# Kernel optimization log

Measured on AMD Instinct MI355X. Metric: run time of the kernel, lower is better.

The kernel has to match this reference:

```python
import math
import jax, jax.numpy as jnp
import numpy as np

NUM_HEADS = 12
EPS = 1e-4


def softmax_kernel_features(data, proj, is_query):
    # data: [B,H,N,d], proj: [m,d] -> features [B,H,N,m]
    d = data.shape[-1]
    data_normalizer = 1.0 / math.sqrt(math.sqrt(d))
    ratio = 1.0 / math.sqrt(proj.shape[0])
    data_dash = jnp.einsum('bhnd,md->bhnm', data_normalizer * data, proj)
    diag_data = (jnp.sum(jnp.square(data), axis=-1, keepdims=True)
                 * 0.5 * data_normalizer * data_normalizer)  # [B,H,N,1]
    if is_query:
        stab = jnp.max(data_dash, axis=-1, keepdims=True)
    else:
        stab = jnp.max(data_dash)
    return ratio * (jnp.exp(data_dash - diag_data - stab) + EPS)


def setup_inputs() -> dict:
    key = jax.random.key(0)
    k0, k1, k2, k3, k4 = jax.random.split(key, 5)
    B, N, C, H = 8, 4096, 768, NUM_HEADS
    hd = C // H
    m = int(hd * math.log(hd))  # 266
    x = jax.random.normal(k0, (B, N, C), dtype=jnp.float32)
    W_qkv = jax.random.normal(k1, (C, 3 * C), dtype=jnp.float32) / math.sqrt(C)
    W_proj = jax.random.normal(k2, (C, C), dtype=jnp.float32) / math.sqrt(C)
    b_proj = jnp.zeros((C,), dtype=jnp.float32)
    proj_mat = jax.random.normal(k3, (m, hd), dtype=jnp.float32)
    return {'x': x, 'W_qkv': W_qkv, 'W_proj': W_proj, 'b_proj': b_proj,
            'proj_mat': proj_mat}


def reference(x, W_qkv, W_proj, b_proj, proj_mat):
    B, N, C = x.shape
    H = NUM_HEADS
    hd = C // H
    qkv = (x @ W_qkv).reshape(B, N, 3, H, hd)
    qkv = jnp.transpose(qkv, (2, 0, 3, 1, 4))  # [3,B,H,N,hd]
    q, k, v = qkv[0], qkv[1], qkv[2]
    q1 = softmax_kernel_features(q, proj_mat, is_query=True)   # [B,H,N,m]
    k1 = softmax_kernel_features(k, proj_mat, is_query=False)  # [B,H,N,m]
    # FAVOR+ non-causal linear attention
    kv = jnp.einsum('bhnm,bhnd->bhmd', k1, v)        # [B,H,m,hd]
    ksum = jnp.sum(k1, axis=2)                        # [B,H,m]
    z = 1.0 / jnp.einsum('bhnm,bhm->bhn', q1, ksum)  # [B,H,N]
    out = jnp.einsum('bhnm,bhmd->bhnd', q1, kv) * z[..., None]
    out = jnp.transpose(out, (0, 2, 1, 3)).reshape(B, N, C)
    return out @ W_proj + b_proj
```

## Files before the change

### kernel.cpp

```cpp
#include <hip/hip_runtime.h>
#include <hip/hip_bf16.h>
#include <math.h>

#define B_ 8
#define N_TOK 4096
#define C_ 768
#define H_ 12
#define HD_ 64
#define M_ 266
#define TC_ 2304
#define BH_ 96
#define ROWS_ 32768

#define M2 288
#define MP 296
#define KVS 72

#define DN 0.35355339059327373f
#define RATIO 0.06131393394849658f
#define FEPS 1e-4f
#define NEG_INF -3.0e38f

typedef __attribute__((ext_vector_type(4))) float f32x4;
typedef __attribute__((ext_vector_type(8))) short bf16x8;

__device__ __forceinline__ float bf2f(unsigned short u) {
  return __uint_as_float(((unsigned int)u) << 16);
}
__device__ __forceinline__ unsigned short f2bf(float f) {
  unsigned int x = __float_as_uint(f);
  unsigned int r = (x + 0x7fffu + ((x >> 16) & 1u)) >> 16;
  return (unsigned short)r;
}

#define GLOAD_LDS16(g, l) \
  __builtin_amdgcn_global_load_lds( \
      (const __attribute__((address_space(1))) void*)(g), \
      (__attribute__((address_space(3))) void*)(l), 16, 0, 0)

__global__ __launch_bounds__(256) void cast_bf16(
    const float* __restrict__ src, unsigned short* __restrict__ dst, int n)
{
  int i = (blockIdx.x * 256 + threadIdx.x) * 4;
  if (i < n) {
    float4 v = *(const float4*)&src[i];
    ushort4 u;
    u.x = f2bf(v.x); u.y = f2bf(v.y); u.z = f2bf(v.z); u.w = f2bf(v.w);
    *(ushort4*)&dst[i] = u;
  }
}

__global__ __launch_bounds__(256) void cast_pbf(
    const float* __restrict__ P, unsigned short* __restrict__ Pbf)
{
  int idx = blockIdx.x * 256 + threadIdx.x;
  if (idx < M2 * 64) {
    int m = idx >> 6;
    Pbf[idx] = (m < M_) ? f2bf(P[idx]) : (unsigned short)0;
  }
}

__global__ __launch_bounds__(256) void transpose_cast(
    const float* __restrict__ src, unsigned short* __restrict__ dst,
    int R, int Ccols)
{
  __shared__ float t[32][33];
  const int c0 = blockIdx.x * 32, r0 = blockIdx.y * 32;
  const int tx = threadIdx.x & 31, ty = threadIdx.x >> 5;
#pragma unroll
  for (int i = 0; i < 32; i += 8)
    t[ty + i][tx] = src[(size_t)(r0 + ty + i) * Ccols + c0 + tx];
  __syncthreads();
#pragma unroll
  for (int i = 0; i < 32; i += 8)
    dst[(size_t)(c0 + ty + i) * R + r0 + tx] = f2bf(t[tx][ty + i]);
}

template <int NT, int C_BF16, int HAS_BIAS>
__global__ __launch_bounds__(512) void gemm_pipe(
    const unsigned short* __restrict__ A, const unsigned short* __restrict__ Bt,
    const float* __restrict__ bias, void* __restrict__ Cptr)
{
  __shared__ unsigned short lds_[73728];
  const int Kdim = 768, Ndim = NT * 128;
  const int tid = threadIdx.x;
  const int lane = tid & 63, w = tid >> 6;

  const int id = blockIdx.x;
  const int sid = (id & 7) * (16 * NT) + (id >> 3);
  const int row0 = (sid / NT) * 256;
  const int col0 = (sid % NT) * 128;

  const int srow = w * 8 + (lane >> 3);
  const int skb = (((lane & 7) ^ ((lane >> 3) & 7)) << 4);
  const size_t agb0 = (size_t)(row0 + srow) * Kdim + (skb >> 1);
  const size_t agb1 = (size_t)(row0 + 64 + srow) * Kdim + (skb >> 1);
  const size_t agb2 = (size_t)(row0 + 128 + srow) * Kdim + (skb >> 1);
  const size_t agb3 = (size_t)(row0 + 192 + srow) * Kdim + (skb >> 1);
  const size_t bgb0 = (size_t)(col0 + srow) * Kdim + (skb >> 1);
  const size_t bgb1 = (size_t)(col0 + 64 + srow) * Kdim + (skb >> 1);
  const int al0 = 0 * 4096 + w * 512 + lane * 8;
  const int al1 = 1 * 4096 + w * 512 + lane * 8;
  const int al2 = 2 * 4096 + w * 512 + lane * 8;
  const int al3 = 3 * 4096 + w * 512 + lane * 8;
  const int bl0 = 16384 + 0 * 4096 + w * 512 + lane * 8;
  const int bl1 = 16384 + 1 * 4096 + w * 512 + lane * 8;

#define STAGE_Q(tt) do { \
    unsigned short* Lq_ = lds_ + ((tt) % 3) * 24576; \
    const int kq_ = (tt) * 64; \
    GLOAD_LDS16(A + agb0 + kq_, Lq_ + al0); \
    GLOAD_LDS16(A + agb1 + kq_, Lq_ + al1); \
    GLOAD_LDS16(A + agb2 + kq_, Lq_ + al2); \
    GLOAD_LDS16(A + agb3 + kq_, Lq_ + al3); \
    GLOAD_LDS16(Bt + bgb0 + kq_, Lq_ + bl0); \
    GLOAD_LDS16(Bt + bgb1 + kq_, Lq_ + bl1); \
  } while (0)

  const int fr = lane & 15, q = lane >> 4;
  const int wm = w >> 2, wn = w & 3;
  const int f7 = fr & 7;
  const int sl0 = ((q + 0) ^ f7) << 3;
  const int sl1 = ((q + 4) ^ f7) << 3;
  const int abase = (wm * 128 + fr) * 64;
  const int bbase0 = 16384 + (wn * 32 + fr) * 64;
  const int bbase1 = 16384 + (wn * 32 + 16 + fr) * 64;

  f32x4 acc[8][2];
  const f32x4 fz = {0.f, 0.f, 0.f, 0.f};
#pragma unroll
  for (int m = 0; m < 8; ++m) { acc[m][0] = fz; acc[m][1] = fz; }

  STAGE_Q(0);
  STAGE_Q(1);

#pragma unroll 1
  for (int t = 0; t < 12; ++t) {
    if (t < 10) STAGE_Q(t + 2);
    if (t < 10)       asm volatile("s_waitcnt vmcnt(12)" ::: "memory");
    else if (t == 10) asm volatile("s_waitcnt vmcnt(6)" ::: "memory");
    else              asm volatile("s_waitcnt vmcnt(0)" ::: "memory");
    __builtin_amdgcn_sched_barrier(0);
    __builtin_amdgcn_s_barrier();
    __builtin_amdgcn_sched_barrier(0);

    const unsigned short* Lb = lds_ + (t % 3) * 24576;
#pragma unroll
    for (int ks = 0; ks < 2; ++ks) {
      const int sl = ks ? sl1 : sl0;
      bf16x8 bv0 = *(const bf16x8*)&Lb[bbase0 + sl];
      bf16x8 bv1 = *(const bf16x8*)&Lb[bbase1 + sl];
      bf16x8 av[8];
#pragma unroll
      for (int m = 0; m < 8; ++m)
        av[m] = *(const bf16x8*)&Lb[abase + m * 1024 + sl];
      __builtin_amdgcn_s_setprio(1);
#pragma unroll
      for (int m = 0; m < 8; ++m) {
        acc[m][0] = __builtin_amdgcn_mfma_f32_16x16x32_bf16(av[m], bv0, acc[m][0], 0, 0, 0);
        acc[m][1] = __builtin_amdgcn_mfma_f32_16x16x32_bf16(av[m], bv1, acc[m][1], 0, 0, 0);
      }
      __builtin_amdgcn_s_setprio(0);
    }
    __builtin_amdgcn_sched_barrier(0);
    __builtin_amdgcn_s_barrier();
    __builtin_amdgcn_sched_barrier(0);
  }
#undef STAGE_Q

  const int orow = q * 4;
#pragma unroll
  for (int m = 0; m < 8; ++m) {
#pragma unroll
    for (int n = 0; n < 2; ++n) {
      const int c = col0 + wn * 32 + n * 16 + fr;
      float badd = 0.f;
      if constexpr (HAS_BIAS) badd = bias[c];
#pragma unroll
      for (int j = 0; j < 4; ++j) {
        const int r = row0 + wm * 128 + m * 16 + orow + j;
        float v = acc[m][n][j] + badd;
        if constexpr (C_BF16)
          ((unsigned short*)Cptr)[(size_t)r * Ndim + c] = f2bf(v);
        else
          ((float*)Cptr)[(size_t)r * Ndim + c] = v;
      }
    }
  }
}

__global__ __launch_bounds__(256) void kmax_mfma(
    const unsigned short* __restrict__ qkv, const unsigned short* __restrict__ Pbf,
    float* __restrict__ bmax)
{
  __shared__ unsigned short K_lds[2][64 * KVS];
  __shared__ float red[4];
  const int tid = threadIdx.x;
  const int w = tid >> 6, lane = tid & 63;
  const int lr = lane & 15, q = lane >> 4;
  const int bh = blockIdx.x, chunk = blockIdx.y;
  const int b = bh / H_, h = bh % H_;
  const int ms = w * 4;
  const int mc = (w == 3) ? 5 : 4;
  const int sn = 16 * w + (lane >> 2);
  const int sd0 = (lane & 3) * 16;
  const f32x4 fz = {0.f, 0.f, 0.f, 0.f};
  float mx = NEG_INF;

  bf16x8 pf0[5], pf1[5];
#pragma unroll
  for (int i = 0; i < 5; ++i) {
    const unsigned short* prow = Pbf + (size_t)((ms + i) * 16 + lr) * 64 + q * 8;
    pf0[i] = *(const bf16x8*)prow;
    pf1[i] = *(const bf16x8*)(prow + 32);
  }

  const unsigned short* kbase = qkv + (size_t)(b * N_TOK + chunk * 512 + sn) * TC_ + C_ + h * HD_ + sd0;
  const size_t gstep = (size_t)64 * TC_;

  int4 ka = *(const int4*)kbase;
  int4 kb = *(const int4*)(kbase + 8);
  *(int4*)&K_lds[0][sn * KVS + sd0] = ka;
  *(int4*)&K_lds[0][sn * KVS + sd0 + 8] = kb;
  asm volatile("s_waitcnt lgkmcnt(0)" ::: "memory");
  __builtin_amdgcn_s_barrier();

#pragma unroll 1
  for (int g = 0; g < 8; ++g) {
    const unsigned short* Kc = K_lds[g & 1];
    if (g < 7) {
      const unsigned short* kr = kbase + (size_t)(g + 1) * gstep;
      ka = *(const int4*)kr;
      kb = *(const int4*)(kr + 8);
    }
    __builtin_amdgcn_sched_barrier(0);
    bf16x8 bk[4][2];
#pragma unroll
    for (int nt = 0; nt < 4; ++nt) {
      bk[nt][0] = *(const bf16x8*)&Kc[(nt * 16 + lr) * KVS + q * 8];
      bk[nt][1] = *(const bf16x8*)&Kc[(nt * 16 + lr) * KVS + 32 + q * 8];
    }
#pragma unroll
    for (int i = 0; i < 5; ++i) {
      if (i >= mc) continue;
      const int m = (ms + i) * 16 + lr;
#pragma unroll
      for (int nt = 0; nt < 4; ++nt) {
        f32x4 s = fz;
        s = __builtin_amdgcn_mfma_f32_16x16x32_bf16(bk[nt][0], pf0[i], s, 0, 0, 0);
        s = __builtin_amdgcn_mfma_f32_16x16x32_bf16(bk[nt][1], pf1[i], s, 0, 0, 0);
        if (m < M_)
          mx = fmaxf(mx, fmaxf(fmaxf(s[0], s[1]), fmaxf(s[2], s[3])));
      }
    }
    if (g < 7) {
      __builtin_amdgcn_sched_barrier(0);
      unsigned short* Kn = (unsigned short*)K_lds[(g & 1) ^ 1];
      *(int4*)&Kn[sn * KVS + sd0] = ka;
      *(int4*)&Kn[sn * KVS + sd0 + 8] = kb;
      asm volatile("s_waitcnt lgkmcnt(0)" ::: "memory");
      __builtin_amdgcn_sched_barrier(0);
      __builtin_amdgcn_s_barrier();
      __builtin_amdgcn_sched_barrier(0);
    }
  }
#pragma unroll
  for (int off = 32; off >= 1; off >>= 1) mx = fmaxf(mx, __shfl_xor(mx, off));
  if (lane == 0) red[w] = mx;
  __syncthreads();
  if (tid == 0)
    bmax[chunk * BH_ + bh] = fmaxf(fmaxf(red[0], red[1]), fmaxf(red[2], red[3]));
}

__global__ __launch_bounds__(256) void kmax_reduce(
    const float* __restrict__ bmax, float* __restrict__ kmaxp, int n)
{
  __shared__ float red[4];
  float v = NEG_INF;
  for (int i = threadIdx.x; i < n; i += 256) v = fmaxf(v, bmax[i]);
#pragma unroll
  for (int off = 32; off >= 1; off >>= 1) v = fmaxf(v, __shfl_xor(v, off));
  if ((threadIdx.x & 63) == 0) red[threadIdx.x >> 6] = v;
  __syncthreads();
  if (threadIdx.x == 0)
    kmaxp[0] = DN * fmaxf(fmaxf(red[0], red[1]), fmaxf(red[2], red[3]));
}

__global__ __launch_bounds__(256) void kv_partial_mfma(
    const unsigned short* __restrict__ qkv, const unsigned short* __restrict__ Pbf,
    const float* __restrict__ kmaxp,
    float* __restrict__ kvpart, float* __restrict__ ksumpart)
{
  __shared__ unsigned short K_lds[2][64 * KVS];
  __shared__ unsigned short Vt_lds[2][64 * KVS];
  __shared__ unsigned short k1_lds[272 * KVS];
  __shared__ float diag_lds[2][64];
  const int tid = threadIdx.x;
  const int w = tid >> 6, lane = tid & 63;
  const int lr = lane & 15, q = lane >> 4;
  const int bh = blockIdx.x, chunk = blockIdx.y;
  const int b = bh / H_, h = bh % H_;
  const float stab = kmaxp[0];
  const int ms = w * 4;
  const int mc = (w == 3) ? 5 : 4;
  const int sn = 16 * w + (lane >> 2);
  const int sd0 = (lane & 3) * 16;
  const f32x4 fz = {0.f, 0.f, 0.f, 0.f};

  f32x4 kvacc[5][4];
  float ksacc[5];
#pragma unroll
  for (int i = 0; i < 5; ++i) {
    ksacc[i] = 0.f;
#pragma unroll
    for (int dt = 0; dt < 4; ++dt) kvacc[i][dt] = fz;
  }

  bf16x8 pf0[5], pf1[5];
#pragma unroll
  for (int i = 0; i < 5; ++i) {
    const unsigned short* prow = Pbf + (size_t)((ms + i) * 16 + lr) * 64 + q * 8;
    pf0[i] = *(const bf16x8*)prow;
    pf1[i] = *(const bf16x8*)(prow + 32);
  }

  const unsigned short* kbase = qkv + (size_t)(b * N_TOK + chunk * 512 + sn) * TC_ + C_ + h * HD_ + sd0;
  const size_t gstep = (size_t)64 * TC_;

  auto write_buf = [&](int bsel, int4 wka, int4 wkb, int4 wva, int4 wvb) {
    *(int4*)&K_lds[bsel][sn * KVS + sd0] = wka;
    *(int4*)&K_lds[bsel][sn * KVS + sd0 + 8] = wkb;
    float sq = 0.f;
    const unsigned short* pk0 = (const unsigned short*)&wka;
#pragma unroll
    for (int j = 0; j < 8; ++j) { float f = bf2f(pk0[j]); sq = fmaf(f, f, sq); }
    const unsigned short* pk1 = (const unsigned short*)&wkb;
#pragma unroll
    for (int j = 0; j < 8; ++j) { float f = bf2f(pk1[j]); sq = fmaf(f, f, sq); }
    sq += __shfl_xor(sq, 1);
    sq += __shfl_xor(sq, 2);
    if ((lane & 3) == 0) diag_lds[bsel][sn] = 0.0625f * sq;
    const unsigned short* pv0 = (const unsigned short*)&wva;
    const unsigned short* pv1 = (const unsigned short*)&wvb;
#pragma unroll
    for (int j = 0; j < 8; ++j) Vt_lds[bsel][(sd0 + j) * KVS + sn] = pv0[j];
#pragma unroll
    for (int j = 0; j < 8; ++j) Vt_lds[bsel][(sd0 + 8 + j) * KVS + sn] = pv1[j];
  };

  int4 ka = *(const int4*)kbase;
  int4 kb = *(const int4*)(kbase + 8);
  int4 va = *(const int4*)(kbase + C_);
  int4 vb = *(const int4*)(kbase + C_ + 8);
  write_buf(0, ka, kb, va, vb);
  asm volatile("s_waitcnt lgkmcnt(0)" ::: "memory");
  __builtin_amdgcn_s_barrier();

#pragma unroll 1
  for (int g = 0; g < 8; ++g) {
    const int cur = g & 1;
    const unsigned short* Kc = K_lds[cur];
    const unsigned short* Vc = Vt_lds[cur];
    const float* Dc = diag_lds[cur];
    if (g < 7) {
      const unsigned short* kr = kbase + (size_t)(g + 1) * gstep;
      ka = *(const int4*)kr;
      kb = *(const int4*)(kr + 8);
      va = *(const int4*)(kr + C_);
      vb = *(const int4*)(kr + C_ + 8);
    }
    __builtin_amdgcn_sched_barrier(0);

    bf16x8 bk[4][2];
#pragma unroll
    for (int nt = 0; nt < 4; ++nt) {
      bk[nt][0] = *(const bf16x8*)&Kc[(nt * 16 + lr) * KVS + q * 8];
      bk[nt][1] = *(const bf16x8*)&Kc[(nt * 16 + lr) * KVS + 32 + q * 8];
    }

#pragma unroll
    for (int i = 0; i < 5; ++i) {
      if (i >= mc) continue;
      const int mt = ms + i;
      const int m = mt * 16 + lr;
      float loc = 0.f;
#pragma unroll
      for (int nt = 0; nt < 4; ++nt) {
        f32x4 s = fz;
        s = __builtin_amdgcn_mfma_f32_16x16x32_bf16(bk[nt][0], pf0[i], s, 0, 0, 0);
        s = __builtin_amdgcn_mfma_f32_16x16x32_bf16(bk[nt][1], pf1[i], s, 0, 0, 0);
        ushort4 uo;
        unsigned short* puo = (unsigned short*)&uo;
#pragma unroll
        for (int j = 0; j < 4; ++j) {
          const int nl = nt * 16 + q * 4 + j;
          float k1f = 0.f;
          if (m < M_) {
            float dash = DN * s[j];
            k1f = RATIO * (__expf(dash - Dc[nl] - stab) + FEPS);
          }
          loc += k1f;
          puo[j] = f2bf(k1f);
        }
        *(ushort4*)&k1_lds[(size_t)(mt * 16 + lr) * KVS + nt * 16 + q * 4] = uo;
      }
      ksacc[i] += loc;
    }
#pragma unroll
    for (int ks = 0; ks < 2; ++ks) {
      bf16x8 bv[4];
#pragma unroll
      for (int dt = 0; dt < 4; ++dt)
        bv[dt] = *(const bf16x8*)&Vc[(dt * 16 + lr) * KVS + ks * 32 + q * 8];
#pragma unroll
      for (int i = 0; i < 5; ++i) {
        if (i >= mc) continue;
        bf16x8 a1 = *(const bf16x8*)&k1_lds[(size_t)((ms + i) * 16 + lr) * KVS + ks * 32 + q * 8];
#pragma unroll
        for (int dt = 0; dt < 4; ++dt)
          kvacc[i][dt] = __builtin_amdgcn_mfma_f32_16x16x32_bf16(a1, bv[dt], kvacc[i][dt], 0, 0, 0);
      }
    }

    if (g < 7) {
      __builtin_amdgcn_sched_barrier(0);
      write_buf(cur ^ 1, ka, kb, va, vb);
      asm volatile("s_waitcnt lgkmcnt(0)" ::: "memory");
      __builtin_amdgcn_sched_barrier(0);
      __builtin_amdgcn_s_barrier();
      __builtin_amdgcn_sched_barrier(0);
    }
  }

  const size_t cb = (size_t)(chunk * BH_ + bh) * 64;
#pragma unroll
  for (int i = 0; i < 5; ++i) {
    if (i >= mc) continue;
    const int mt = ms + i;
#pragma unroll
    for (int dt = 0; dt < 4; ++dt) {
      float4 v4;
      v4.x = kvacc[i][dt][0]; v4.y = kvacc[i][dt][1];
      v4.z = kvacc[i][dt][2]; v4.w = kvacc[i][dt][3];
      *(float4*)&kvpart[(cb + dt * 16 + lr) * M2 + mt * 16 + q * 4] = v4;
    }
    float s = ksacc[i];
    s += __shfl_xor(s, 16);
    s += __shfl_xor(s, 32);
    if (lane < 16)
      ksumpart[(size_t)(chunk * BH_ + bh) * M2 + mt * 16 + lane] = s;
  }
}

__global__ __launch_bounds__(256) void kv_reduce2(
    const float* __restrict__ kvpart, const float* __restrict__ ksumpart,
    unsigned short* __restrict__ kvt_g, float* __restrict__ ksum_g)
{
  const int KVN = BH_ * 64 * M2;
  const int KSN = BH_ * M2;
  int idx = blockIdx.x * 256 + threadIdx.x;
  if (idx < KVN) {
    int m = idx % M2;
    float s = 0.f;
    if (m < M_) {
#pragma unroll
      for (int c = 0; c < 8; ++c) s += kvpart[(size_t)c * KVN + idx];
    }
    kvt_g[idx] = f2bf(s);
  } else if (idx < KVN + KSN) {
    int j = idx - KVN;
    int m = j % M2;
    float s = 0.f;
    if (m < M_) {
#pragma unroll
      for (int c = 0; c < 8; ++c) s += ksumpart[(size_t)c * KSN + j];
    }
    ksum_g[j] = s;
  }
}

__global__ __launch_bounds__(256) void attn_mfma(
    const unsigned short* __restrict__ qkv, const unsigned short* __restrict__ Pbf,
    const unsigned short* __restrict__ kvt_g, const float* __restrict__ ksum_g,
    unsigned short* __restrict__ attn)
{
  __shared__ unsigned short q1_lds[64 * MP];
  __shared__ unsigned short kvt_lds[64 * MP];
  __shared__ float ksum_lds[M2];
  __shared__ float z_lds[64];
  const int tid = threadIdx.x;
  const int bh = blockIdx.x, qt = blockIdx.y;
  const int b = bh / H_, h = bh % H_;
  const int n0 = qt * 64;
  const int w = tid >> 6, lane = tid & 63;
  const int lr = lane & 15, q = lane >> 4;

  {
    const unsigned short* src = kvt_g + (size_t)bh * 64 * M2;
#pragma unroll
    for (int i = 0; i < 9; ++i) {
      int chunk = i * 256 + tid;
      int r = chunk / 36, c = (chunk % 36) * 8;
      *(int4*)&kvt_lds[r * MP + c] = *(const int4*)(src + r * M2 + c);
    }
    if (tid < 72)
      *(float4*)&ksum_lds[tid * 4] = *(const float4*)(ksum_g + (size_t)bh * M2 + tid * 4);
    if (tid < 64) {
      const int4 z4 = {0, 0, 0, 0};
      *(int4*)&q1_lds[tid * MP + 272] = z4;
      *(int4*)&q1_lds[tid * MP + 280] = z4;
    }
  }
  __syncthreads();

  const unsigned short* qrow = qkv + (size_t)(b * N_TOK + n0 + w * 16 + lr) * TC_ + h * HD_;
  bf16x8 bq0 = *(const bf16x8*)(qrow + q * 8);
  bf16x8 bq1 = *(const bf16x8*)(qrow + q * 8 + 32);
  float sq = 0.f;
  {
    const unsigned short* p0 = (const unsigned short*)&bq0;
    const unsigned short* p1 = (const unsigned short*)&bq1;
#pragma unroll
    for (int j = 0; j < 8; ++j) { float f = bf2f(p0[j]); sq = fmaf(f, f, sq); }
#pragma unroll
    for (int j = 0; j < 8; ++j) { float f = bf2f(p1[j]); sq = fmaf(f, f, sq); }
  }
  sq += __shfl_xor(sq, 16);
  sq += __shfl_xor(sq, 32);
  const float diag = 0.0625f * sq;

  f32x4 sacc[17];
  const f32x4 fz = {0.f, 0.f, 0.f, 0.f};
#pragma unroll
  for (int mt = 0; mt < 17; ++mt) sacc[mt] = fz;
#pragma unroll
  for (int mt = 0; mt < 17; ++mt) {
    const unsigned short* prow = Pbf + (size_t)(mt * 16 + lr) * 64;
    bf16x8 ap0 = *(const bf16x8*)(prow + q * 8);
    bf16x8 ap1 = *(const bf16x8*)(prow + q * 8 + 32);
    sacc[mt] = __builtin_amdgcn_mfma_f32_16x16x32_bf16(ap0, bq0, sacc[mt], 0, 0, 0);
    sacc[mt] = __builtin_amdgcn_mfma_f32_16x16x32_bf16(ap1, bq1, sacc[mt], 0, 0, 0);
  }

  float mxr = NEG_INF;
#pragma unroll
  for (int mt = 0; mt < 17; ++mt) {
#pragma unroll
    for (int j = 0; j < 4; ++j) {
      int m = mt * 16 + q * 4 + j;
      if (m < M_) mxr = fmaxf(mxr, sacc[mt][j]);
    }
  }
  mxr = fmaxf(mxr, __shfl_xor(mxr, 16));
  mxr = fmaxf(mxr, __shfl_xor(mxr, 32));
  const float mxd = DN * mxr;

  float zp = 0.f;
#pragma unroll
  for (int mt = 0; mt < 17; ++mt) {
    ushort4 uo;
    unsigned short* puo = (unsigned short*)&uo;
#pragma unroll
    for (int j = 0; j < 4; ++j) {
      const int m = mt * 16 + q * 4 + j;
      float q1f = 0.f;
      if (m < M_) {
        float dash = DN * sacc[mt][j];
        q1f = RATIO * (__expf(dash - diag - mxd) + FEPS);
      }
      zp = fmaf(q1f, ksum_lds[m], zp);
      puo[j] = f2bf(q1f);
    }
    *(ushort4*)&q1_lds[(w * 16 + lr) * MP + mt * 16 + q * 4] = uo;
  }
  zp += __shfl_xor(zp, 16);
  zp += __shfl_xor(zp, 32);
  if (q == 0) z_lds[w * 16 + lr] = 1.0f / zp;

  f32x4 oacc[4];
#pragma unroll
  for (int dt = 0; dt < 4; ++dt) oacc[dt] = fz;
#pragma unroll
  for (int ks = 0; ks < 9; ++ks) {
    bf16x8 aq = *(const bf16x8*)&q1_lds[(w * 16 + lr) * MP + ks * 32 + q * 8];
#pragma unroll
    for (int dt = 0; dt < 4; ++dt) {
      bf16x8 bkv = *(const bf16x8*)&kvt_lds[(dt * 16 + lr) * MP + ks * 32 + q * 8];
      oacc[dt] = __builtin_amdgcn_mfma_f32_16x16x32_bf16(aq, bkv, oacc[dt], 0, 0, 0);
    }
  }

  float zz[4];
#pragma unroll
  for (int j = 0; j < 4; ++j) zz[j] = z_lds[w * 16 + q * 4 + j];
#pragma unroll
  for (int dt = 0; dt < 4; ++dt) {
#pragma unroll
    for (int j = 0; j < 4; ++j) {
      const int r = b * N_TOK + n0 + w * 16 + q * 4 + j;
      attn[(size_t)r * C_ + h * HD_ + dt * 16 + lr] = f2bf(oacc[dt][j] * zz[j]);
    }
  }
}

extern "C" void kernel_launch(void* const* d_in, const int* in_sizes, int n_in,
                              void* d_out, int out_size, void* d_ws, size_t ws_size,
                              hipStream_t stream) {
  const float* x     = (const float*)d_in[0];
  const float* Wqkv  = (const float*)d_in[1];
  const float* Wproj = (const float*)d_in[2];
  const float* bproj = (const float*)d_in[3];
  const float* P     = (const float*)d_in[4];
  float* out = (float*)d_out;
  float* ws = (float*)d_ws;

  unsigned short* qkv    = (unsigned short*)ws;
  unsigned short* xb     = (unsigned short*)(ws + 37748736);
  float*          kvpart = ws + 37748736;
  unsigned short* attn   = (unsigned short*)(ws + 37748736);
  float* ksumpart = ws + 51904512;
  unsigned short* kvt_g  = (unsigned short*)(ws + 52125696);
  float* ksum_g   = ws + 53010432;
  float* bmax     = ws + 53038080;
  float* kmaxp    = ws + 53041152;
  unsigned short* Pbf    = (unsigned short*)(ws + 53041216);
  unsigned short* Wqkvt  = (unsigned short*)(ws + 53050432);
  unsigned short* Wprojt = (unsigned short*)(ws + 53935168);

  cast_bf16<<<dim3(24576), 256, 0, stream>>>(x, xb, ROWS_ * C_);
  transpose_cast<<<dim3(72, 24), 256, 0, stream>>>(Wqkv, Wqkvt, C_, TC_);
  transpose_cast<<<dim3(24, 24), 256, 0, stream>>>(Wproj, Wprojt, C_, C_);
  cast_pbf<<<dim3(72), 256, 0, stream>>>(P, Pbf);

  gemm_pipe<18, 1, 0><<<dim3(2304), 512, 0, stream>>>(xb, Wqkvt, nullptr, qkv);
  kmax_mfma<<<dim3(96, 8), 256, 0, stream>>>(qkv, Pbf, bmax);
  kmax_reduce<<<dim3(1), 256, 0, stream>>>(bmax, kmaxp, 768);
  kv_partial_mfma<<<dim3(96, 8), 256, 0, stream>>>(qkv, Pbf, kmaxp, kvpart, ksumpart);
  kv_reduce2<<<dim3(7020), 256, 0, stream>>>(kvpart, ksumpart, kvt_g, ksum_g);
  attn_mfma<<<dim3(96, 64), 256, 0, stream>>>(qkv, Pbf, kvt_g, ksum_g, attn);
  gemm_pipe<6, 0, 1><<<dim3(768), 512, 0, stream>>>(attn, Wprojt, bproj, out);
}
```

Measured before the change: 557.8 us.

## Interleave k1 feature compute with kv MFMA per 32-token slice and shrink LDS

Restructures kv_partial_mfma so each 32-token slice computes k1 features and immediately feeds them into the kv MFMAs. The k1 staging buffer shrinks to a 32-column tile, the K/V double buffers become single buffers with an extra barrier before refilling, and XOR swizzles are added on the transposed V writes and k1 tile to avoid LDS bank conflicts. This cuts LDS footprint, which may raise occupancy, and reduces bank conflicts. In exchange it adds a barrier per iteration and loses overlap between the LDS refill and compute.

```diff
diff --git a/kernel.cpp b/kernel.cpp
--- a/kernel.cpp
+++ b/kernel.cpp
@@ -15,6 +15,7 @@
 #define M2 288
 #define MP 296
 #define KVS 72
+#define K1S 40
 
 #define DN 0.35355339059327373f
 #define RATIO 0.06131393394849658f
@@ -291,10 +292,10 @@
     const float* __restrict__ kmaxp,
     float* __restrict__ kvpart, float* __restrict__ ksumpart)
 {
-  __shared__ unsigned short K_lds[2][64 * KVS];
-  __shared__ unsigned short Vt_lds[2][64 * KVS];
-  __shared__ unsigned short k1_lds[272 * KVS];
-  __shared__ float diag_lds[2][64];
+  __shared__ unsigned short K_lds[64 * KVS];
+  __shared__ unsigned short Vt_lds[64 * KVS];
+  __shared__ unsigned short k1_lds[272 * K1S];
+  __shared__ float diag_lds[64];
   const int tid = threadIdx.x;
   const int w = tid >> 6, lane = tid & 63;
   const int lr = lane & 15, q = lane >> 4;
@@ -305,6 +306,8 @@
   const int mc = (w == 3) ? 5 : 4;
   const int sn = 16 * w + (lane >> 2);
   const int sd0 = (lane & 3) * 16;
+  const int vswz = sn ^ ((lane & 3) << 4);
+  const int kswz = (lr >> 3) << 4;
   const f32x4 fz = {0.f, 0.f, 0.f, 0.f};
 
   f32x4 kvacc[5][4];
@@ -327,9 +330,9 @@
   const unsigned short* kbase = qkv + (size_t)(b * N_TOK + chunk * 512 + sn) * TC_ + C_ + h * HD_ + sd0;
   const size_t gstep = (size_t)64 * TC_;
 
-  auto write_buf = [&](int bsel, int4 wka, int4 wkb, int4 wva, int4 wvb) {
-    *(int4*)&K_lds[bsel][sn * KVS + sd0] = wka;
-    *(int4*)&K_lds[bsel][sn * KVS + sd0 + 8] = wkb;
+  auto write_buf = [&](int4 wka, int4 wkb, int4 wva, int4 wvb) {
+    *(int4*)&K_lds[sn * KVS + sd0] = wka;
+    *(int4*)&K_lds[sn * KVS + sd0 + 8] = wkb;
     float sq = 0.f;
     const unsigned short* pk0 = (const unsigned short*)&wka;
 #pragma unroll
@@ -339,29 +342,25 @@
     for (int j = 0; j < 8; ++j) { float f = bf2f(pk1[j]); sq = fmaf(f, f, sq); }
     sq += __shfl_xor(sq, 1);
     sq += __shfl_xor(sq, 2);
-    if ((lane & 3) == 0) diag_lds[bsel][sn] = 0.0625f * sq;
+    if ((lane & 3) == 0) diag_lds[sn] = 0.0625f * sq;
     const unsigned short* pv0 = (const unsigned short*)&wva;
     const unsigned short* pv1 = (const unsigned short*)&wvb;
 #pragma unroll
-    for (int j = 0; j < 8; ++j) Vt_lds[bsel][(sd0 + j) * KVS + sn] = pv0[j];
-#pragma unroll
-    for (int j = 0; j < 8; ++j) Vt_lds[bsel][(sd0 + 8 + j) * KVS + sn] = pv1[j];
+    for (int j = 0; j < 8; ++j) Vt_lds[(sd0 + j) * KVS + vswz] = pv0[j];
+#pragma unroll
+    for (int j = 0; j < 8; ++j) Vt_lds[(sd0 + 8 + j) * KVS + vswz] = pv1[j];
   };
 
   int4 ka = *(const int4*)kbase;
   int4 kb = *(const int4*)(kbase + 8);
   int4 va = *(const int4*)(kbase + C_);
   int4 vb = *(const int4*)(kbase + C_ + 8);
-  write_buf(0, ka, kb, va, vb);
+  write_buf(ka, kb, va, vb);
   asm volatile("s_waitcnt lgkmcnt(0)" ::: "memory");
   __builtin_amdgcn_s_barrier();
 
 #pragma unroll 1
   for (int g = 0; g < 8; ++g) {
-    const int cur = g & 1;
-    const unsigned short* Kc = K_lds[cur];
-    const unsigned short* Vc = Vt_lds[cur];
-    const float* Dc = diag_lds[cur];
     if (g < 7) {
       const unsigned short* kr = kbase + (size_t)(g + 1) * gstep;
       ka = *(const int4*)kr;
@@ -371,51 +370,49 @@
     }
     __builtin_amdgcn_sched_barrier(0);
 
-    bf16x8 bk[4][2];
-#pragma unroll
-    for (int nt = 0; nt < 4; ++nt) {
-      bk[nt][0] = *(const bf16x8*)&Kc[(nt * 16 + lr) * KVS + q * 8];
-      bk[nt][1] = *(const bf16x8*)&Kc[(nt * 16 + lr) * KVS + 32 + q * 8];
-    }
-
-#pragma unroll
-    for (int i = 0; i < 5; ++i) {
-      if (i >= mc) continue;
-      const int mt = ms + i;
-      const int m = mt * 16 + lr;
-      float loc = 0.f;
-#pragma unroll
-      for (int nt = 0; nt < 4; ++nt) {
-        f32x4 s = fz;
-        s = __builtin_amdgcn_mfma_f32_16x16x32_bf16(bk[nt][0], pf0[i], s, 0, 0, 0);
-        s = __builtin_amdgcn_mfma_f32_16x16x32_bf16(bk[nt][1], pf1[i], s, 0, 0, 0);
-        ushort4 uo;
-        unsigned short* puo = (unsigned short*)&uo;
-#pragma unroll
-        for (int j = 0; j < 4; ++j) {
-          const int nl = nt * 16 + q * 4 + j;
-          float k1f = 0.f;
-          if (m < M_) {
-            float dash = DN * s[j];
-            k1f = RATIO * (__expf(dash - Dc[nl] - stab) + FEPS);
-          }
-          loc += k1f;
-          puo[j] = f2bf(k1f);
-        }
-        *(ushort4*)&k1_lds[(size_t)(mt * 16 + lr) * KVS + nt * 16 + q * 4] = uo;
+#pragma unroll
+    for (int ks = 0; ks < 2; ++ks) {
+      bf16x8 bkl[2][2];
+#pragma unroll
+      for (int t = 0; t < 2; ++t) {
+        const int nrow = ((2 * ks + t) * 16 + lr) * KVS;
+        bkl[t][0] = *(const bf16x8*)&K_lds[nrow + q * 8];
+        bkl[t][1] = *(const bf16x8*)&K_lds[nrow + 32 + q * 8];
       }
-      ksacc[i] += loc;
-    }
-#pragma unroll
-    for (int ks = 0; ks < 2; ++ks) {
       bf16x8 bv[4];
 #pragma unroll
       for (int dt = 0; dt < 4; ++dt)
-        bv[dt] = *(const bf16x8*)&Vc[(dt * 16 + lr) * KVS + ks * 32 + q * 8];
+        bv[dt] = *(const bf16x8*)&Vt_lds[(dt * 16 + lr) * KVS + ((ks * 32 + q * 8) ^ (dt << 4))];
+
 #pragma unroll
       for (int i = 0; i < 5; ++i) {
         if (i >= mc) continue;
-        bf16x8 a1 = *(const bf16x8*)&k1_lds[(size_t)((ms + i) * 16 + lr) * KVS + ks * 32 + q * 8];
+        const int mt = ms + i;
+        const int m = mt * 16 + lr;
+        const int mrow = (mt * 16 + lr) * K1S;
+        float loc = 0.f;
+#pragma unroll
+        for (int t = 0; t < 2; ++t) {
+          f32x4 s = fz;
+          s = __builtin_amdgcn_mfma_f32_16x16x32_bf16(bkl[t][0], pf0[i], s, 0, 0, 0);
+          s = __builtin_amdgcn_mfma_f32_16x16x32_bf16(bkl[t][1], pf1[i], s, 0, 0, 0);
+          ushort4 uo;
+          unsigned short* puo = (unsigned short*)&uo;
+#pragma unroll
+          for (int j = 0; j < 4; ++j) {
+            const int nl = (2 * ks + t) * 16 + q * 4 + j;
+            float k1f = 0.f;
+            if (m < M_) {
+              float dash = DN * s[j];
+              k1f = RATIO * (__expf(dash - diag_lds[nl] - stab) + FEPS);
+            }
+            loc += k1f;
+            puo[j] = f2bf(k1f);
+          }
+          *(ushort4*)&k1_lds[mrow + ((t * 16 + q * 4) ^ kswz)] = uo;
+        }
+        ksacc[i] += loc;
+        bf16x8 a1 = *(const bf16x8*)&k1_lds[mrow + ((q * 8) ^ kswz)];
 #pragma unroll
         for (int dt = 0; dt < 4; ++dt)
           kvacc[i][dt] = __builtin_amdgcn_mfma_f32_16x16x32_bf16(a1, bv[dt], kvacc[i][dt], 0, 0, 0);
@@ -424,7 +421,9 @@
 
     if (g < 7) {
       __builtin_amdgcn_sched_barrier(0);
-      write_buf(cur ^ 1, ka, kb, va, vb);
+      __builtin_amdgcn_s_barrier();
+      __builtin_amdgcn_sched_barrier(0);
+      write_buf(ka, kb, va, vb);
       asm volatile("s_waitcnt lgkmcnt(0)" ::: "memory");
       __builtin_amdgcn_sched_barrier(0);
       __builtin_amdgcn_s_barrier();
```

Measured after the change: 562.4 us. No clear change (+0.8%).
